# Kernel optimization log

Hardware: AMD Instinct MI355X
Metric: run time of the kernel (lower is better)

## Reference

```python
import jax, jax.numpy as jnp
import numpy as np

B, U, L, H, M = 4, 16, 128, 768, 256   # docs, utterances/doc, tokens/utt, hidden, mentions/doc
HID = 150                               # Score MLP hidden dim
N_CLUSTERS = 32


def setup_inputs() -> dict:
    key = jax.random.key(0)
    ks = jax.random.split(key, 8)
    hidden = jax.random.normal(ks[0], (B, U, L, H), jnp.float32)

    rng = np.random.default_rng(0)
    span_utt = rng.integers(0, U, (B, M))
    span_start = rng.integers(0, L - 8, (B, M))
    span_end = span_start + rng.integers(1, 9, (B, M))  # span length in [1, 8]

    # coreference labels: label[i, j] = 1 iff j is a true antecedent (j < i, same cluster);
    # if mention i has no antecedent, label[i, i] = 1 (the epsilon / new-entity slot).
    clusters = rng.integers(0, N_CLUSTERS, (B, M))
    same = clusters[:, :, None] == clusters[:, None, :]
    ant = same & np.tril(np.ones((M, M), bool), -1)
    labels = ant.astype(np.float32)
    diag = np.arange(M)
    labels[:, diag, diag] = (~ant.any(-1)).astype(np.float32)

    scale = 0.02
    W1 = jax.random.normal(ks[1], (3 * H, HID), jnp.float32) * scale
    W2 = jax.random.normal(ks[2], (HID, HID), jnp.float32) * scale
    W3 = jax.random.normal(ks[3], (HID, 1), jnp.float32) * scale
    return {
        "hidden": hidden,
        "span_utt": jnp.asarray(span_utt, jnp.int32),
        "span_start": jnp.asarray(span_start, jnp.int32),
        "span_end": jnp.asarray(span_end, jnp.int32),
        "labels": jnp.asarray(labels),
        "W1": W1, "b1": jnp.zeros((HID,), jnp.float32),
        "W2": W2, "b2": jnp.zeros((HID,), jnp.float32),
        "W3": W3, "b3": jnp.zeros((1,), jnp.float32),
    }


def reference(hidden, span_utt, span_start, span_end, labels, W1, b1, W2, b2, W3, b3):
    # ---- span mean-pooling (EntityEncoder, aggr='mean') ----
    pos = jnp.arange(L)
    mask = (pos[None, None, :] >= span_start[..., None]) & (pos[None, None, :] < span_end[..., None])
    w = mask.astype(hidden.dtype) / (span_end - span_start)[..., None].astype(hidden.dtype)  # [B,M,L]
    gathered = jnp.take_along_axis(hidden, span_utt[:, :, None, None], axis=1)  # [B,M,L,H]
    pooled = jnp.einsum('bml,bmlh->bmh', w, gathered)  # [B,M,H]

    # ---- pairwise antecedent scoring (PairScorer / Score MLP, dropout=eval) ----
    ii, jj = np.tril_indices(M, -1)  # static pair indices, P = M(M-1)/2
    # concat(i_g, j_g, i_g*j_g) @ W1  ==  i_g@W1a + j_g@W1b + (i_g*j_g)@W1c
    W1a, W1b, W1c = W1[:H], W1[H:2 * H], W1[2 * H:]
    hi = pooled @ W1a   # [B,M,HID]
    hj = pooled @ W1b   # [B,M,HID]
    prod = pooled[:, ii] * pooled[:, jj]                    # [B,P,H]
    h1 = jax.nn.relu(hi[:, ii] + hj[:, jj] + prod @ W1c + b1)
    h2 = jax.nn.relu(h1 @ W2 + b2)
    s = (h2 @ W3 + b3)[..., 0]  # [B,P]

    # ---- per-mention ragged softmax, padded to [M, M] with -1000 ----
    # row i has logits s_ij for j<i plus epsilon=0 at j=i (diagonal of zeros matrix)
    logits = jnp.zeros((B, M, M), hidden.dtype).at[:, ii, jj].set(s)
    valid = jnp.tril(jnp.ones((M, M), bool))
    probs = jax.nn.softmax(jnp.where(valid, logits, -1e30), axis=-1)
    probs = jnp.where(valid, probs, jnp.asarray(-1000.0, hidden.dtype))

    # ---- compute_loss ----
    eps = 1e-8
    prob_sum = jnp.sum(jnp.clip(probs * labels, eps, 1.0 - eps), axis=-1)  # [B,M]
    loss = -jnp.sum(jnp.log(prob_sum))
    return loss
```

## Files before the change

kernel.cpp:

```cpp
#include <hip/hip_runtime.h>
#include <hip/hip_bf16.h>

#define B_ 4
#define U_ 16
#define L_ 128
#define H_ 768
#define M_ 256
#define HID_ 150

typedef _Float16 half8 __attribute__((ext_vector_type(8)));
typedef _Float16 half4t __attribute__((ext_vector_type(4)));
typedef float floatx4 __attribute__((ext_vector_type(4)));
typedef float floatx16 __attribute__((ext_vector_type(16)));

__device__ __forceinline__ void gl_lds16(const _Float16* g, _Float16* l)
{
    __builtin_amdgcn_global_load_lds(
        (const __attribute__((address_space(1))) unsigned int*)g,
        (__attribute__((address_space(3))) unsigned int*)l, 16, 0, 0);
}

__global__ __launch_bounds__(256) void prep_pool_kernel(
    const float* __restrict__ W1, const float* __restrict__ W2,
    const float* __restrict__ b2, const float* __restrict__ W3,
    const float* __restrict__ hidden, const int* __restrict__ sutt,
    const int* __restrict__ sstart, const int* __restrict__ send,
    _Float16* __restrict__ W1cs, _Float16* __restrict__ W2s,
    _Float16* __restrict__ W1abs, float2* __restrict__ bw,
    _Float16* __restrict__ pooledh)
{
    if (blockIdx.x >= 1540) {
        const int bm = (blockIdx.x - 1540) * 4 + (threadIdx.x >> 6);
        const int lane = threadIdx.x & 63;
        const int b  = bm >> 8;
        const int u  = sutt[bm];
        const int st = sstart[bm];
        const int en = send[bm];
        const float inv = 1.0f / (float)(en - st);
        const float* src = hidden + ((size_t)(b * U_ + u) * L_) * H_ + lane * 12;
        float4 s[3];
        #pragma unroll
        for (int q = 0; q < 3; ++q) s[q] = make_float4(0.f, 0.f, 0.f, 0.f);
        for (int l = st; l < en; ++l) {
            const float* p = src + (size_t)l * H_;
            #pragma unroll
            for (int q = 0; q < 3; ++q) {
                float4 v = *(const float4*)(p + q * 4);
                s[q].x += v.x; s[q].y += v.y; s[q].z += v.z; s[q].w += v.w;
            }
        }
        _Float16* gp = pooledh + (size_t)bm * H_ + lane * 12;
        #pragma unroll
        for (int q = 0; q < 3; ++q) {
            half4t hv;
            hv[0] = (_Float16)(s[q].x * inv); hv[1] = (_Float16)(s[q].y * inv);
            hv[2] = (_Float16)(s[q].z * inv); hv[3] = (_Float16)(s[q].w * inv);
            *(half4t*)(gp + q * 4) = hv;
        }
        return;
    }
    int idx = blockIdx.x * 256 + threadIdx.x;
    if (blockIdx.x == 0 && threadIdx.x < 160) {
        int n = threadIdx.x;
        bw[n] = (n < HID_) ? make_float2(b2[n], W3[n]) : make_float2(0.f, 0.f);
    }
    if (idx < 122880) {
        int k = idx / 160, n = idx - k * 160;
        float v = (n < HID_) ? W1[(size_t)(2 * H_ + k) * HID_ + n] : 0.f;
        W1cs[(k >> 4) * 2560 + (n >> 5) * 512 +
             (((n & 31) | (((k >> 3) & 1) << 5)) << 3) + (k & 7)] = (_Float16)v;
        return;
    }
    idx -= 122880;
    if (idx < 25600) {
        int k = idx / 160, n = idx - k * 160;
        float v = (k < HID_ && n < HID_) ? W2[(size_t)k * HID_ + n] : 0.f;
        W2s[(k >> 4) * 2560 + (n >> 5) * 512 +
            (((n & 31) | (((k >> 3) & 1) << 5)) << 3) + (k & 7)] = (_Float16)v;
        return;
    }
    idx -= 25600;
    if (idx < 245760) {
        int k = idx / 320, n = idx - k * 320;
        float v = 0.f;
        if (n < HID_) v = W1[(size_t)k * HID_ + n];
        else if (n >= 160 && n < 160 + HID_) v = W1[(size_t)(H_ + k) * HID_ + (n - 160)];
        W1abs[(k >> 5) * 10240 + (n >> 4) * 512 +
              (((n & 15) | (((k >> 3) & 3) << 4)) << 3) + (k & 7)] = (_Float16)v;
    }
}

__global__ __launch_bounds__(256) void hihj_kernel(
    const _Float16* __restrict__ pooledh, const float* __restrict__ b1,
    const _Float16* __restrict__ W1abs,
    float* __restrict__ hiF, float* __restrict__ hjT,
    _Float16* __restrict__ pjF)
{
    if (blockIdx.x >= 64) {
        const int idx = (blockIdx.x - 64) * 256 + threadIdx.x;
        const int g = idx / 3072, rem = idx - g * 3072;
        const int kc = rem >> 7, rem2 = rem & 127;
        const int chunk = rem2 >> 6, l = rem2 & 63;
        const int row = (g >> 3) * 256 + (g & 7) * 32 + (l & 31);
        const int col = kc * 32 + chunk * 16 + ((l >> 5) << 3);
        *(half8*)&pjF[(size_t)idx * 8] =
            *(const half8*)&pooledh[(size_t)row * H_ + col];
        return;
    }
    __shared__ __align__(16) _Float16 spool[16 * 776];
    const int blk = blockIdx.x;
    const int tid = threadIdx.x;
    for (int e = tid; e < 16 * 96; e += 256) {
        int r = e / 96, c = e - r * 96;
        *(half8*)&spool[r * 776 + c * 8] =
            *(const half8*)&pooledh[(size_t)(blk * 16 + r) * H_ + c * 8];
    }
    __syncthreads();

    const int w = tid >> 6, lane = tid & 63;
    const int g = lane >> 4, l15 = lane & 15;
    floatx4 acc[5];
    #pragma unroll
    for (int u5 = 0; u5 < 5; ++u5) acc[u5] = (floatx4){0.f, 0.f, 0.f, 0.f};
    const _Float16* aB = &spool[l15 * 776 + g * 8];
    for (int kc = 0; kc < 24; ++kc) {
        half8 av = *(const half8*)(aB + kc * 32);
        #pragma unroll
        for (int u5 = 0; u5 < 5; ++u5) {
            const int u = w * 5 + u5;
            half8 bv = *(const half8*)(W1abs + (size_t)((kc * 20 + u) * 64 + lane) * 8);
            acc[u5] = __builtin_amdgcn_mfma_f32_16x16x32_f16(av, bv, acc[u5], 0, 0, 0);
        }
    }
    const int row0 = blk * 16 + g * 4;
    #pragma unroll
    for (int u5 = 0; u5 < 5; ++u5) {
        const int n = (w * 5 + u5) * 16 + l15;
        if (n < HID_) {
            float b1v = b1[n];
            #pragma unroll
            for (int r = 0; r < 4; ++r)
                hiF[(size_t)(row0 + r) * 160 + n] = acc[u5][r] + b1v;
        } else if (n >= 160 && n < 160 + HID_) {
            *(float4*)&hjT[(size_t)(n - 160) * 1024 + row0] =
                make_float4(acc[u5][0], acc[u5][1], acc[u5][2], acc[u5][3]);
        }
    }
}

__global__ __launch_bounds__(128, 3) void pair_mlp_kernel(
    const _Float16* __restrict__ pooledh, const _Float16* __restrict__ pjF,
    const float* __restrict__ hiF, const float* __restrict__ hjT,
    const _Float16* __restrict__ W1cs, const _Float16* __restrict__ W2s,
    const float2* __restrict__ bw, const float* __restrict__ b3,
    float* __restrict__ logits)
{
    __shared__ __align__(16) _Float16 smem[2 * 5440];

    int q = blockIdx.x;
    const int b = q / 576;
    int r = q - b * 576;
    int jt = 0;
    while (r >= 128 - 16 * jt) { r -= 128 - 16 * jt; ++jt; }
    const int p = 16 * jt + r;
    const int i0 = 2 * p, j0 = jt * 32;
    const int bm = b * M_;
    const int w = threadIdx.x >> 6;
    const int lane = threadIdx.x & 63;
    const int c31 = lane & 31;
    const int hw = lane >> 5;

    _Float16* Wb0 = smem;
    _Float16* Wb1 = smem + 5120;
    _Float16* h1w = smem + w * 5440;

    const _Float16* pjb = pjF + (size_t)(b * 8 + jt) * 24576 + lane * 8;
    const _Float16* pip = pooledh + (size_t)(bm + i0 + w) * H_ + (hw << 3);

    floatx16 acc1[5];
    #pragma unroll
    for (int t1 = 0; t1 < 5; ++t1)
        #pragma unroll
        for (int e = 0; e < 16; ++e) acc1[t1][e] = 0.f;

    {
        const _Float16* gW = W1cs + (size_t)(5 * w) * 512 + lane * 8;
        #pragma unroll
        for (int c = 0; c < 5; ++c)
            gl_lds16(gW + c * 512, Wb0 + (5 * w + c) * 512);
    }
    half8 Apj0 = *(const half8*)(pjb);
    half8 Apj1 = *(const half8*)(pjb + 512);
    half8 Ai0  = *(const half8*)(pip);
    half8 Ai1  = *(const half8*)(pip + 16);
    __syncthreads();

    for (int kc = 0; kc < 24; ++kc) {
        const _Float16* Wcur = (kc & 1) ? Wb1 : Wb0;
        _Float16*       Wnxt = (kc & 1) ? Wb0 : Wb1;
        half8 npj0, npj1, ni0, ni1;
        if (kc < 23) {
            const _Float16* gW = W1cs + (size_t)(kc + 1) * 5120 + (5 * w) * 512 + lane * 8;
            #pragma unroll
            for (int c = 0; c < 5; ++c)
                gl_lds16(gW + c * 512, Wnxt + (5 * w + c) * 512);
            npj0 = *(const half8*)(pjb + (kc + 1) * 1024);
            npj1 = *(const half8*)(pjb + (kc + 1) * 1024 + 512);
            const int kb = (kc + 1) * 32;
            ni0  = *(const half8*)(pip + kb);
            ni1  = *(const half8*)(pip + kb + 16);
        }
        {
            half8 a = Ai0 * Apj0;
            #pragma unroll
            for (int t1 = 0; t1 < 5; ++t1) {
                half8 wf = *(const half8*)&Wcur[t1 * 512 + lane * 8];
                acc1[t1] = __builtin_amdgcn_mfma_f32_32x32x16_f16(wf, a, acc1[t1], 0, 0, 0);
            }
        }
        {
            half8 a = Ai1 * Apj1;
            #pragma unroll
            for (int t1 = 0; t1 < 5; ++t1) {
                half8 wf = *(const half8*)&Wcur[(5 + t1) * 512 + lane * 8];
                acc1[t1] = __builtin_amdgcn_mfma_f32_32x32x16_f16(wf, a, acc1[t1], 0, 0, 0);
            }
        }
        if (kc < 23) { Apj0 = npj0; Apj1 = npj1; Ai0 = ni0; Ai1 = ni1; }
        __syncthreads();
    }

    const int jcol = bm + j0 + c31;
    #pragma unroll
    for (int t1 = 0; t1 < 5; ++t1) {
        #pragma unroll
        for (int qd = 0; qd < 4; ++qd) {
            const int n1 = t1 * 32 + 8 * qd + 4 * hw;
            float hj0 = hjT[(size_t)(n1 + 0) * 1024 + jcol];
            float hj1 = hjT[(size_t)(n1 + 1) * 1024 + jcol];
            float hj2 = hjT[(size_t)(n1 + 2) * 1024 + jcol];
            float hj3 = hjT[(size_t)(n1 + 3) * 1024 + jcol];
            float4 hiv = *(const float4*)&hiF[(size_t)(bm + i0 + w) * 160 + n1];
            half4t hv;
            hv[0] = (_Float16)fmaxf(acc1[t1][4 * qd + 0] + hiv.x + hj0, 0.f);
            hv[1] = (_Float16)fmaxf(acc1[t1][4 * qd + 1] + hiv.y + hj1, 0.f);
            hv[2] = (_Float16)fmaxf(acc1[t1][4 * qd + 2] + hiv.z + hj2, 0.f);
            hv[3] = (_Float16)fmaxf(acc1[t1][4 * qd + 3] + hiv.w + hj3, 0.f);
            *(half4t*)&h1w[c31 * 170 + n1] = hv;
        }
    }
    __syncthreads();

    const float b3v = b3[0];
    floatx16 acc2[5];
    #pragma unroll
    for (int t2 = 0; t2 < 5; ++t2)
        #pragma unroll
        for (int e = 0; e < 16; ++e) acc2[t2][e] = 0.f;

    half8 W2b[2][5], h1b[2];
    #pragma unroll
    for (int c = 0; c < 2; ++c) {
        const _Float16* wb = W2s + (size_t)(c * 5) * 512 + lane * 8;
        #pragma unroll
        for (int t2 = 0; t2 < 5; ++t2) W2b[c][t2] = *(const half8*)(wb + t2 * 512);
        h1b[c] = *(const half8*)&h1w[c31 * 170 + c * 16 + hw * 8];
    }
    for (int kc2 = 0; kc2 < 10; ++kc2) {
        const int cur = kc2 & 1;
        half8 nw[5], nh;
        if (kc2 < 8) {
            const _Float16* wb = W2s + (size_t)((kc2 + 2) * 5) * 512 + lane * 8;
            #pragma unroll
            for (int t2 = 0; t2 < 5; ++t2) nw[t2] = *(const half8*)(wb + t2 * 512);
            nh = *(const half8*)&h1w[c31 * 170 + (kc2 + 2) * 16 + hw * 8];
        }
        #pragma unroll
        for (int t2 = 0; t2 < 5; ++t2)
            acc2[t2] = __builtin_amdgcn_mfma_f32_32x32x16_f16(
                W2b[cur][t2], h1b[cur], acc2[t2], 0, 0, 0);
        if (kc2 < 8) {
            #pragma unroll
            for (int t2 = 0; t2 < 5; ++t2) W2b[cur][t2] = nw[t2];
            h1b[cur] = nh;
        }
    }

    float sown = 0.f;
    #pragma unroll
    for (int t2 = 0; t2 < 5; ++t2) {
        #pragma unroll
        for (int qd = 0; qd < 4; ++qd) {
            const int n2 = t2 * 32 + 8 * qd + 4 * hw;
            float4 bw01 = *(const float4*)&bw[n2];
            float4 bw23 = *(const float4*)&bw[n2 + 2];
            sown += fmaxf(acc2[t2][4 * qd + 0] + bw01.x, 0.f) * bw01.y;
            sown += fmaxf(acc2[t2][4 * qd + 1] + bw01.z, 0.f) * bw01.w;
            sown += fmaxf(acc2[t2][4 * qd + 2] + bw23.x, 0.f) * bw23.y;
            sown += fmaxf(acc2[t2][4 * qd + 3] + bw23.z, 0.f) * bw23.w;
        }
    }
    float s = sown + __shfl_xor(sown, 32);
    const int i = i0 + w;
    const int j = j0 + c31;
    if (lane < 32 && j < i)
        logits[(size_t)(bm + i) * M_ + j] = s + b3v;
}

__global__ __launch_bounds__(64) void loss_kernel(
    const float* __restrict__ logits, const float* __restrict__ labels,
    float* __restrict__ out)
{
    const int bm = blockIdx.x;
    const int i  = bm & (M_ - 1);
    const int lane = threadIdx.x;

    float val[4];
    #pragma unroll
    for (int qq = 0; qq < 4; ++qq) {
        const int j = qq * 64 + lane;
        val[qq] = (j < i) ? logits[(size_t)bm * M_ + j]
                          : ((j == i) ? 0.0f : -1e30f);
    }
    float m = fmaxf(fmaxf(val[0], val[1]), fmaxf(val[2], val[3]));
    #pragma unroll
    for (int off = 32; off >= 1; off >>= 1) m = fmaxf(m, __shfl_xor(m, off));

    float s = 0.f;
    float e[4];
    #pragma unroll
    for (int qq = 0; qq < 4; ++qq) {
        const int j = qq * 64 + lane;
        e[qq] = (j <= i) ? expf(val[qq] - m) : 0.0f;
        s += e[qq];
    }
    #pragma unroll
    for (int off = 32; off >= 1; off >>= 1) s += __shfl_xor(s, off);
    const float inv_s = 1.0f / s;

    float rs = 0.f;
    #pragma unroll
    for (int qq = 0; qq < 4; ++qq) {
        const int j = qq * 64 + lane;
        float prob = (j <= i) ? (e[qq] * inv_s) : -1000.0f;
        float tv = prob * labels[(size_t)bm * M_ + j];
        rs += fminf(fmaxf(tv, 1e-8f), 1.0f - 1e-8f);
    }
    #pragma unroll
    for (int off = 32; off >= 1; off >>= 1) rs += __shfl_xor(rs, off);

    if (lane == 0) atomicAdd(out, -logf(rs));
}

extern "C" void kernel_launch(void* const* d_in, const int* in_sizes, int n_in,
                              void* d_out, int out_size, void* d_ws, size_t ws_size,
                              hipStream_t stream)
{
    const float* hidden = (const float*)d_in[0];
    const int*   sutt   = (const int*)d_in[1];
    const int*   sstart = (const int*)d_in[2];
    const int*   send   = (const int*)d_in[3];
    const float* labels = (const float*)d_in[4];
    const float* W1     = (const float*)d_in[5];
    const float* b1     = (const float*)d_in[6];
    const float* W2     = (const float*)d_in[7];
    const float* b2     = (const float*)d_in[8];
    const float* W3     = (const float*)d_in[9];
    const float* b3     = (const float*)d_in[10];

    float* ws = (float*)d_ws;
    float*    hiF     = ws;
    float*    hjT     = ws + 163840;
    float*    logits  = ws + 327680;
    float2*   bw      = (float2*)(ws + 589824);
    _Float16* pooledh = (_Float16*)(ws + 590144);
    _Float16* W1cs    = (_Float16*)(ws + 983360);
    _Float16* W2s     = (_Float16*)(ws + 1106240);
    _Float16* W1abs   = (_Float16*)(ws + 1119040);
    _Float16* pjF     = (_Float16*)(ws + 1241920);
    float* out = (float*)d_out;

    hipMemsetAsync(d_out, 0, sizeof(float), stream);

    prep_pool_kernel<<<dim3(1796), 256, 0, stream>>>(
        W1, W2, b2, W3, hidden, sutt, sstart, send,
        W1cs, W2s, W1abs, bw, pooledh);
    hihj_kernel<<<dim3(448), 256, 0, stream>>>(pooledh, b1, W1abs,
                                               hiF, hjT, pjF);
    pair_mlp_kernel<<<dim3(576 * B_), 128, 0, stream>>>(pooledh, pjF, hiF, hjT,
                                                        W1cs, W2s, bw, b3, logits);
    loss_kernel<<<dim3(B_ * M_), 64, 0, stream>>>(logits, labels, out);
}
```

Measured before the change: 192.6 us.

## Switch pair MLP to 16x16x32 MFMA with four waves per block

Pair MLP blocks now run 256 threads (4 waves), and each wave handles one i-row and 16 j-columns using 16x16x32 f16 MFMAs instead of 32x32x16. The W1c, W2 and pj staging layouts are rewritten to match the 16-wide fragment format. The aim is more waves per block and a smaller accumulator footprint (40 vs 80 registers), giving better occupancy and latency hiding. The cost is more MFMA instructions per unit of work, per-wave reloads of W2 from global memory, and an extra shuffle in the final reduction.

After: 190.5 us (median of 2 runs). No clear change (-1.1%).

```diff
diff --git a/kernel.cpp b/kernel.cpp
--- a/kernel.cpp
+++ b/kernel.cpp
@@ -11,7 +11,6 @@
 typedef _Float16 half8 __attribute__((ext_vector_type(8)));
 typedef _Float16 half4t __attribute__((ext_vector_type(4)));
 typedef float floatx4 __attribute__((ext_vector_type(4)));
-typedef float floatx16 __attribute__((ext_vector_type(16)));
 
 __device__ __forceinline__ void gl_lds16(const _Float16* g, _Float16* l)
 {
@@ -25,7 +24,7 @@
     const float* __restrict__ b2, const float* __restrict__ W3,
     const float* __restrict__ hidden, const int* __restrict__ sutt,
     const int* __restrict__ sstart, const int* __restrict__ send,
-    _Float16* __restrict__ W1cs, _Float16* __restrict__ W2s,
+    _Float16* __restrict__ W1cs16, _Float16* __restrict__ W2s16,
     _Float16* __restrict__ W1abs, float2* __restrict__ bw,
     _Float16* __restrict__ pooledh)
 {
@@ -67,16 +66,16 @@
     if (idx < 122880) {
         int k = idx / 160, n = idx - k * 160;
         float v = (n < HID_) ? W1[(size_t)(2 * H_ + k) * HID_ + n] : 0.f;
-        W1cs[(k >> 4) * 2560 + (n >> 5) * 512 +
-             (((n & 31) | (((k >> 3) & 1) << 5)) << 3) + (k & 7)] = (_Float16)v;
+        W1cs16[((k >> 5) * 10 + (n >> 4)) * 512 +
+               (((n & 15) | (((k >> 3) & 3) << 4)) << 3) + (k & 7)] = (_Float16)v;
         return;
     }
     idx -= 122880;
     if (idx < 25600) {
         int k = idx / 160, n = idx - k * 160;
         float v = (k < HID_ && n < HID_) ? W2[(size_t)k * HID_ + n] : 0.f;
-        W2s[(k >> 4) * 2560 + (n >> 5) * 512 +
-            (((n & 31) | (((k >> 3) & 1) << 5)) << 3) + (k & 7)] = (_Float16)v;
+        W2s16[((k >> 5) * 10 + (n >> 4)) * 512 +
+              (((n & 15) | (((k >> 3) & 3) << 4)) << 3) + (k & 7)] = (_Float16)v;
         return;
     }
     idx -= 25600;
@@ -94,16 +93,15 @@
     const _Float16* __restrict__ pooledh, const float* __restrict__ b1,
     const _Float16* __restrict__ W1abs,
     float* __restrict__ hiF, float* __restrict__ hjT,
-    _Float16* __restrict__ pjF)
+    _Float16* __restrict__ pjF16)
 {
     if (blockIdx.x >= 64) {
         const int idx = (blockIdx.x - 64) * 256 + threadIdx.x;
-        const int g = idx / 3072, rem = idx - g * 3072;
-        const int kc = rem >> 7, rem2 = rem & 127;
-        const int chunk = rem2 >> 6, l = rem2 & 63;
-        const int row = (g >> 3) * 256 + (g & 7) * 32 + (l & 31);
-        const int col = kc * 32 + chunk * 16 + ((l >> 5) << 3);
-        *(half8*)&pjF[(size_t)idx * 8] =
+        const int g16 = idx / 1536, rem = idx - g16 * 1536;
+        const int kc = rem >> 6, l = rem & 63;
+        const int row = (g16 >> 4) * 256 + (g16 & 15) * 16 + (l & 15);
+        const int col = kc * 32 + ((l >> 4) << 3);
+        *(half8*)&pjF16[(size_t)idx * 8] =
             *(const half8*)&pooledh[(size_t)row * H_ + col];
         return;
     }
@@ -148,14 +146,14 @@
     }
 }
 
-__global__ __launch_bounds__(128, 3) void pair_mlp_kernel(
-    const _Float16* __restrict__ pooledh, const _Float16* __restrict__ pjF,
+__global__ __launch_bounds__(256, 4) void pair_mlp_kernel(
+    const _Float16* __restrict__ pooledh, const _Float16* __restrict__ pjF16,
     const float* __restrict__ hiF, const float* __restrict__ hjT,
-    const _Float16* __restrict__ W1cs, const _Float16* __restrict__ W2s,
+    const _Float16* __restrict__ W1cs16, const _Float16* __restrict__ W2s16,
     const float2* __restrict__ bw, const float* __restrict__ b3,
     float* __restrict__ logits)
 {
-    __shared__ __align__(16) _Float16 smem[2 * 5440];
+    __shared__ __align__(16) _Float16 smem[10880];
 
     int q = blockIdx.x;
     const int b = q / 576;
@@ -166,144 +164,105 @@
     const int i0 = 2 * p, j0 = jt * 32;
     const int bm = b * M_;
     const int w = threadIdx.x >> 6;
+    const int iw = w >> 1, jh = w & 1;
+    const int i = i0 + iw;
     const int lane = threadIdx.x & 63;
-    const int c31 = lane & 31;
-    const int hw = lane >> 5;
+    const int l15 = lane & 15;
+    const int g4 = lane >> 4;
 
     _Float16* Wb0 = smem;
     _Float16* Wb1 = smem + 5120;
-    _Float16* h1w = smem + w * 5440;
-
-    const _Float16* pjb = pjF + (size_t)(b * 8 + jt) * 24576 + lane * 8;
-    const _Float16* pip = pooledh + (size_t)(bm + i0 + w) * H_ + (hw << 3);
-
-    floatx16 acc1[5];
-    #pragma unroll
-    for (int t1 = 0; t1 < 5; ++t1)
-        #pragma unroll
-        for (int e = 0; e < 16; ++e) acc1[t1][e] = 0.f;
-
-    {
-        const _Float16* gW = W1cs + (size_t)(5 * w) * 512 + lane * 8;
+    _Float16* h1w = smem + w * 2720;
+
+    const _Float16* pjb = pjF16 + (size_t)(b * 16 + jt * 2 + jh) * 12288 + lane * 8;
+    const _Float16* pip = pooledh + (size_t)(bm + i) * H_ + (g4 << 3);
+
+    floatx4 acc1[10];
+    #pragma unroll
+    for (int t = 0; t < 10; ++t) acc1[t] = (floatx4){0.f, 0.f, 0.f, 0.f};
+
+    if (w < 2) {
+        const _Float16* gW = W1cs16 + (size_t)(5 * w) * 512 + lane * 8;
         #pragma unroll
         for (int c = 0; c < 5; ++c)
             gl_lds16(gW + c * 512, Wb0 + (5 * w + c) * 512);
     }
-    half8 Apj0 = *(const half8*)(pjb);
-    half8 Apj1 = *(const half8*)(pjb + 512);
-    half8 Ai0  = *(const half8*)(pip);
-    half8 Ai1  = *(const half8*)(pip + 16);
+    half8 Apj = *(const half8*)(pjb);
+    half8 Api = *(const half8*)(pip);
     __syncthreads();
 
     for (int kc = 0; kc < 24; ++kc) {
         const _Float16* Wcur = (kc & 1) ? Wb1 : Wb0;
         _Float16*       Wnxt = (kc & 1) ? Wb0 : Wb1;
-        half8 npj0, npj1, ni0, ni1;
+        half8 npj, npi;
         if (kc < 23) {
-            const _Float16* gW = W1cs + (size_t)(kc + 1) * 5120 + (5 * w) * 512 + lane * 8;
-            #pragma unroll
-            for (int c = 0; c < 5; ++c)
-                gl_lds16(gW + c * 512, Wnxt + (5 * w + c) * 512);
-            npj0 = *(const half8*)(pjb + (kc + 1) * 1024);
-            npj1 = *(const half8*)(pjb + (kc + 1) * 1024 + 512);
-            const int kb = (kc + 1) * 32;
-            ni0  = *(const half8*)(pip + kb);
-            ni1  = *(const half8*)(pip + kb + 16);
-        }
-        {
-            half8 a = Ai0 * Apj0;
-            #pragma unroll
-            for (int t1 = 0; t1 < 5; ++t1) {
-                half8 wf = *(const half8*)&Wcur[t1 * 512 + lane * 8];
-                acc1[t1] = __builtin_amdgcn_mfma_f32_32x32x16_f16(wf, a, acc1[t1], 0, 0, 0);
+            if (w < 2) {
+                const _Float16* gW = W1cs16 + (size_t)(kc + 1) * 5120
+                                     + (5 * w) * 512 + lane * 8;
+                #pragma unroll
+                for (int c = 0; c < 5; ++c)
+                    gl_lds16(gW + c * 512, Wnxt + (5 * w + c) * 512);
             }
-        }
-        {
-            half8 a = Ai1 * Apj1;
-            #pragma unroll
-            for (int t1 = 0; t1 < 5; ++t1) {
-                half8 wf = *(const half8*)&Wcur[(5 + t1) * 512 + lane * 8];
-                acc1[t1] = __builtin_amdgcn_mfma_f32_32x32x16_f16(wf, a, acc1[t1], 0, 0, 0);
-            }
-        }
-        if (kc < 23) { Apj0 = npj0; Apj1 = npj1; Ai0 = ni0; Ai1 = ni1; }
+            npj = *(const half8*)(pjb + (kc + 1) * 512);
+            npi = *(const half8*)(pip + (kc + 1) * 32);
+        }
+        half8 a = Api * Apj;
+        #pragma unroll
+        for (int t = 0; t < 10; ++t) {
+            half8 wf = *(const half8*)&Wcur[t * 512 + lane * 8];
+            acc1[t] = __builtin_amdgcn_mfma_f32_16x16x32_f16(wf, a, acc1[t], 0, 0, 0);
+        }
+        if (kc < 23) { Apj = npj; Api = npi; }
         __syncthreads();
     }
 
-    const int jcol = bm + j0 + c31;
-    #pragma unroll
-    for (int t1 = 0; t1 < 5; ++t1) {
-        #pragma unroll
-        for (int qd = 0; qd < 4; ++qd) {
-            const int n1 = t1 * 32 + 8 * qd + 4 * hw;
-            float hj0 = hjT[(size_t)(n1 + 0) * 1024 + jcol];
-            float hj1 = hjT[(size_t)(n1 + 1) * 1024 + jcol];
-            float hj2 = hjT[(size_t)(n1 + 2) * 1024 + jcol];
-            float hj3 = hjT[(size_t)(n1 + 3) * 1024 + jcol];
-            float4 hiv = *(const float4*)&hiF[(size_t)(bm + i0 + w) * 160 + n1];
-            half4t hv;
-            hv[0] = (_Float16)fmaxf(acc1[t1][4 * qd + 0] + hiv.x + hj0, 0.f);
-            hv[1] = (_Float16)fmaxf(acc1[t1][4 * qd + 1] + hiv.y + hj1, 0.f);
-            hv[2] = (_Float16)fmaxf(acc1[t1][4 * qd + 2] + hiv.z + hj2, 0.f);
-            hv[3] = (_Float16)fmaxf(acc1[t1][4 * qd + 3] + hiv.w + hj3, 0.f);
-            *(half4t*)&h1w[c31 * 170 + n1] = hv;
-        }
+    const int j = j0 + jh * 16 + l15;
+    const int jcol = bm + j;
+    #pragma unroll
+    for (int t = 0; t < 10; ++t) {
+        const int nb = t * 16 + (g4 << 2);
+        float hj0 = hjT[(size_t)(nb + 0) * 1024 + jcol];
+        float hj1 = hjT[(size_t)(nb + 1) * 1024 + jcol];
+        float hj2 = hjT[(size_t)(nb + 2) * 1024 + jcol];
+        float hj3 = hjT[(size_t)(nb + 3) * 1024 + jcol];
+        float4 hiv = *(const float4*)&hiF[(size_t)(bm + i) * 160 + nb];
+        half4t hv;
+        hv[0] = (_Float16)fmaxf(acc1[t][0] + hiv.x + hj0, 0.f);
+        hv[1] = (_Float16)fmaxf(acc1[t][1] + hiv.y + hj1, 0.f);
+        hv[2] = (_Float16)fmaxf(acc1[t][2] + hiv.z + hj2, 0.f);
+        hv[3] = (_Float16)fmaxf(acc1[t][3] + hiv.w + hj3, 0.f);
+        *(half4t*)&h1w[l15 * 170 + nb] = hv;
     }
     __syncthreads();
 
     const float b3v = b3[0];
-    floatx16 acc2[5];
-    #pragma unroll
-    for (int t2 = 0; t2 < 5; ++t2)
-        #pragma unroll
-        for (int e = 0; e < 16; ++e) acc2[t2][e] = 0.f;
-
-    half8 W2b[2][5], h1b[2];
-    #pragma unroll
-    for (int c = 0; c < 2; ++c) {
-        const _Float16* wb = W2s + (size_t)(c * 5) * 512 + lane * 8;
-        #pragma unroll
-        for (int t2 = 0; t2 < 5; ++t2) W2b[c][t2] = *(const half8*)(wb + t2 * 512);
-        h1b[c] = *(const half8*)&h1w[c31 * 170 + c * 16 + hw * 8];
-    }
-    for (int kc2 = 0; kc2 < 10; ++kc2) {
-        const int cur = kc2 & 1;
-        half8 nw[5], nh;
-        if (kc2 < 8) {
-            const _Float16* wb = W2s + (size_t)((kc2 + 2) * 5) * 512 + lane * 8;
-            #pragma unroll
-            for (int t2 = 0; t2 < 5; ++t2) nw[t2] = *(const half8*)(wb + t2 * 512);
-            nh = *(const half8*)&h1w[c31 * 170 + (kc2 + 2) * 16 + hw * 8];
-        }
-        #pragma unroll
-        for (int t2 = 0; t2 < 5; ++t2)
-            acc2[t2] = __builtin_amdgcn_mfma_f32_32x32x16_f16(
-                W2b[cur][t2], h1b[cur], acc2[t2], 0, 0, 0);
-        if (kc2 < 8) {
-            #pragma unroll
-            for (int t2 = 0; t2 < 5; ++t2) W2b[cur][t2] = nw[t2];
-            h1b[cur] = nh;
+    floatx4 acc2[10];
+    #pragma unroll
+    for (int t2 = 0; t2 < 10; ++t2) acc2[t2] = (floatx4){0.f, 0.f, 0.f, 0.f};
+    for (int kc2 = 0; kc2 < 5; ++kc2) {
+        half8 hb = *(const half8*)&h1w[l15 * 170 + kc2 * 32 + (g4 << 3)];
+        #pragma unroll
+        for (int t2 = 0; t2 < 10; ++t2) {
+            half8 wf = *(const half8*)(W2s16 + (size_t)(kc2 * 10 + t2) * 512 + lane * 8);
+            acc2[t2] = __builtin_amdgcn_mfma_f32_16x16x32_f16(wf, hb, acc2[t2], 0, 0, 0);
         }
     }
 
     float sown = 0.f;
     #pragma unroll
-    for (int t2 = 0; t2 < 5; ++t2) {
-        #pragma unroll
-        for (int qd = 0; qd < 4; ++qd) {
-            const int n2 = t2 * 32 + 8 * qd + 4 * hw;
-            float4 bw01 = *(const float4*)&bw[n2];
-            float4 bw23 = *(const float4*)&bw[n2 + 2];
-            sown += fmaxf(acc2[t2][4 * qd + 0] + bw01.x, 0.f) * bw01.y;
-            sown += fmaxf(acc2[t2][4 * qd + 1] + bw01.z, 0.f) * bw01.w;
-            sown += fmaxf(acc2[t2][4 * qd + 2] + bw23.x, 0.f) * bw23.y;
-            sown += fmaxf(acc2[t2][4 * qd + 3] + bw23.z, 0.f) * bw23.w;
-        }
-    }
-    float s = sown + __shfl_xor(sown, 32);
-    const int i = i0 + w;
-    const int j = j0 + c31;
-    if (lane < 32 && j < i)
+    for (int t2 = 0; t2 < 10; ++t2) {
+        const int n2 = t2 * 16 + (g4 << 2);
+        float4 bw01 = *(const float4*)&bw[n2];
+        float4 bw23 = *(const float4*)&bw[n2 + 2];
+        sown += fmaxf(acc2[t2][0] + bw01.x, 0.f) * bw01.y;
+        sown += fmaxf(acc2[t2][1] + bw01.z, 0.f) * bw01.w;
+        sown += fmaxf(acc2[t2][2] + bw23.x, 0.f) * bw23.y;
+        sown += fmaxf(acc2[t2][3] + bw23.z, 0.f) * bw23.w;
+    }
+    float s = sown;
+    s += __shfl_xor(s, 16);
+    s += __shfl_xor(s, 32);
+    if (lane < 16 && j < i)
         logits[(size_t)(bm + i) * M_ + j] = s + b3v;
 }
 
@@ -374,20 +333,20 @@
     float*    logits  = ws + 327680;
     float2*   bw      = (float2*)(ws + 589824);
     _Float16* pooledh = (_Float16*)(ws + 590144);
-    _Float16* W1cs    = (_Float16*)(ws + 983360);
-    _Float16* W2s     = (_Float16*)(ws + 1106240);
+    _Float16* W1cs16  = (_Float16*)(ws + 983360);
+    _Float16* W2s16   = (_Float16*)(ws + 1106240);
     _Float16* W1abs   = (_Float16*)(ws + 1119040);
-    _Float16* pjF     = (_Float16*)(ws + 1241920);
+    _Float16* pjF16   = (_Float16*)(ws + 1241920);
     float* out = (float*)d_out;
 
     hipMemsetAsync(d_out, 0, sizeof(float), stream);
 
     prep_pool_kernel<<<dim3(1796), 256, 0, stream>>>(
         W1, W2, b2, W3, hidden, sutt, sstart, send,
-        W1cs, W2s, W1abs, bw, pooledh);
+        W1cs16, W2s16, W1abs, bw, pooledh);
     hihj_kernel<<<dim3(448), 256, 0, stream>>>(pooledh, b1, W1abs,
-                                               hiF, hjT, pjF);
-    pair_mlp_kernel<<<dim3(576 * B_), 128, 0, stream>>>(pooledh, pjF, hiF, hjT,
-                                                        W1cs, W2s, bw, b3, logits);
+                                               hiF, hjT, pjF16);
+    pair_mlp_kernel<<<dim3(576 * B_), 256, 0, stream>>>(pooledh, pjF16, hiF, hjT,
+                                                        W1cs16, W2s16, bw, b3, logits);
     loss_kernel<<<dim3(B_ * M_), 64, 0, stream>>>(logits, labels, out);
 }
```
